# Kernel tuning notes

Hardware: AMD Instinct MI355X
Metric: run time of the kernel (lower is better)

The kernel has to match this reference:

```python
import jax, jax.numpy as jnp
import numpy as np

N = 2048
D_T = 256; D_F = 256
E_T = 32; E_F = 32; E_C = 128
C = 5; Q = 512


def setup_inputs() -> dict:
    key = jax.random.key(0)
    ks = jax.random.split(key, 12)
    # full graph minus self-loops, row-major (matches dense_to_sparse ordering)
    r, c = np.meshgrid(np.arange(N), np.arange(N), indexing='ij')
    m = r != c
    edge_index = jnp.asarray(np.stack([r[m], c[m]]), dtype=jnp.int32)  # [2, N*(N-1)]
    E = edge_index.shape[1]
    s = 0.02
    return {
        'time_features': jax.random.normal(ks[0], (N, D_T), jnp.float32),
        'edge_index': edge_index,
        'time_edge_weight': jax.random.uniform(ks[1], (E,), jnp.float32),
        'freq_features': jax.random.normal(ks[2], (N, D_F), jnp.float32),
        'freq_edge_weight': jax.random.uniform(ks[3], (E,), jnp.float32),
        'labels': jax.random.randint(ks[4], (N,), 0, C, jnp.int32),
        'num_classes': C,
        'query_size': Q,
        'Wt': jax.random.normal(ks[5], (D_T, E_T), jnp.float32) * s,
        'bt': jnp.zeros((E_T,), jnp.float32),
        'Wf': jax.random.normal(ks[6], (D_F, E_F), jnp.float32) * s,
        'bf': jnp.zeros((E_F,), jnp.float32),
        'Wc': jax.random.normal(ks[7], (E_T + E_F + C, E_C), jnp.float32) * s,
        'bc': jnp.zeros((E_C,), jnp.float32),
        'Wo': jax.random.normal(ks[8], (E_C, C), jnp.float32) * s,
        'bo': jnp.zeros((C,), jnp.float32),
    }


def _gcn(x, A, W, b):
    # torch_geometric GCNConv: D^{-1/2}(A + I)D^{-1/2} (X W) + b
    n = A.shape[0]
    Ah = A + jnp.eye(n, dtype=A.dtype)
    deg = Ah.sum(axis=1)
    dis = jnp.where(deg > 0, jax.lax.rsqrt(deg), 0.0)
    return (dis[:, None] * Ah * dis[None, :]) @ (x @ W) + b


def reference(time_features, edge_index, time_edge_weight, freq_features,
              freq_edge_weight, labels, num_classes, query_size,
              Wt, bt, Wf, bf, Wc, bc, Wo, bo):
    n = time_features.shape[0]
    lrelu = lambda z: jax.nn.leaky_relu(z, 0.01)

    def dense_adj(w):  # A[dst, src] = w
        return jnp.zeros((n, n), w.dtype).at[edge_index[1], edge_index[0]].add(w)

    te = lrelu(_gcn(time_features, dense_adj(time_edge_weight), Wt, bt))
    fe = lrelu(_gcn(freq_features, dense_adj(freq_edge_weight), Wf, bf))

    # to_one_hot: one_hot[:n - query_size, labels] = 1 -> support rows get 1 in
    # every column that appears anywhere in `labels`
    cols = jnp.zeros((num_classes,), te.dtype).at[labels].set(1.0)
    rowmask = (jnp.arange(n) < (n - query_size)).astype(te.dtype)
    one_hot = rowmask[:, None] * cols[None, :]

    feats = jnp.concatenate([te, fe, one_hot], axis=-1)  # [n, E_T+E_F+C]

    # graph_construction (no_grad in original): 1 / (L1 distance over the
    # non-one-hot dims + 1e-5), zero diagonal
    fd = jax.lax.stop_gradient(feats[:, : feats.shape[1] - num_classes])
    dist = jnp.sum(jnp.abs(fd[:, None, :] - fd[None, :, :]), axis=-1)  # [n, n]
    Aw = (1.0 / (dist + 1e-5)) * (1.0 - jnp.eye(n, dtype=feats.dtype))

    emb = lrelu(_gcn(feats, Aw, Wc, bc))
    return emb @ Wo + bo
```

## Files before the change

### kernel.cpp

```cpp
#include <hip/hip_runtime.h>
#include <hip/hip_bf16.h>

#define N 2048
#define NM1 2047
#define DT 256
#define ET 32
#define EC 128
#define NC 5
#define FS 80
#define FD 69
#define KC_ET 16
#define KC_EC 16

typedef __hip_bfloat16 bf16;

__global__ __launch_bounds__(256) void k_deg_label_xw(const float* __restrict__ tw,
                                                      const float* __restrict__ fw,
                                                      const int* __restrict__ labels,
                                                      const float* __restrict__ Xt,
                                                      const float* __restrict__ Wt,
                                                      const float* __restrict__ Xf,
                                                      const float* __restrict__ Wf,
                                                      float* __restrict__ degT,
                                                      float* __restrict__ degF,
                                                      float* __restrict__ cols,
                                                      float* __restrict__ Yt,
                                                      float* __restrict__ Yf){
    int b = blockIdx.x;
    int t = threadIdx.x;
    if (b < 512){
        int p = (b & 7)*256 + t;
        if (p >= NM1) return;
        int s0 = (b >> 3)*32;
        float lowT=0.f, highT=0.f, lowF=0.f, highF=0.f;
        #pragma unroll 8
        for (int r = 0; r < 32; ++r){
            int s = s0 + r;
            float vt = tw[(size_t)s*NM1 + p];
            float vf = fw[(size_t)s*NM1 + p];
            if (s <= p){ highT += vt; highF += vf; }
            else       { lowT  += vt; lowF  += vf; }
        }
        atomicAdd(&degT[p],   lowT);
        atomicAdd(&degF[p],   lowF);
        atomicAdd(&degT[p+1], highT);
        atomicAdd(&degF[p+1], highF);
        return;
    }
    if (b == 512){
        __shared__ float lc[NC];
        if (t < NC) lc[t] = 0.f;
        __syncthreads();
        for (int i = t; i < N; i += 256){
            int l = labels[i];
            if (l >= 0 && l < NC) lc[l] = 1.f;
        }
        __syncthreads();
        if (t < NC) cols[t] = lc[t];
        return;
    }
    int idx = b - 513;
    const float* X = (idx & 256) ? Xf : Xt;
    const float* W = (idx & 256) ? Wf : Wt;
    float*       Y = (idx & 256) ? Yf : Yt;
    __shared__ float Ws[DT*ET];
    __shared__ float Xs[8*DT];
    for (int j = t; j < DT*ET; j += 256) Ws[j] = W[j];
    int i0 = (idx & 255)*8;
    for (int j = t; j < 8*DT; j += 256) Xs[j] = X[(size_t)i0*DT + j];
    __syncthreads();
    int r = t >> 5, f = t & 31;
    const float* xr = Xs + r*DT;
    float acc = 0.f;
    #pragma unroll 8
    for (int d = 0; d < DT; ++d) acc += xr[d]*Ws[d*ET+f];
    Y[(size_t)(i0+r)*ET+f] = acc;
}

__global__ __launch_bounds__(256) void k_agg_et(const float* __restrict__ tw,
                                                const float* __restrict__ fw,
                                                const float* __restrict__ Yt,
                                                const float* __restrict__ Yf,
                                                const float* __restrict__ degT,
                                                const float* __restrict__ degF,
                                                float* __restrict__ Pt,
                                                float* __restrict__ Pf){
    __shared__ float Ast[64*68];
    __shared__ float Asf[64*68];
    __shared__ float Zst[64*ET];
    __shared__ float Zsf[64*ET];
    int t = threadIdx.x;
    int i0 = blockIdx.x*64;
    int kc = blockIdx.y;
    int k0 = kc*128;
    int g  = t >> 7;
    int tt = t & 127;
    int ig = tt >> 3, fg = tt & 7;
    int r0 = ig*4, c0 = fg*4;
    const float* As = g ? Asf : Ast;
    const float* Zs = g ? Zsf : Zst;
    float acc[4][4];
    #pragma unroll
    for (int u=0;u<4;++u)
        #pragma unroll
        for (int v=0;v<4;++v) acc[u][v]=0.f;

    for (int kt = 0; kt < 2; ++kt){
        int kb = k0 + kt*64;
        #pragma unroll
        for (int e = 0; e < 16; ++e){
            int id = t + e*256;
            int k_l = id >> 6, i_l = id & 63;
            int k = kb + k_l;
            int gi = i0 + i_l;
            float vt, vf;
            if (gi == k){ vt = 0.f; vf = 0.f; }
            else {
                size_t base = (size_t)k*NM1 + gi - (gi > k ? 1 : 0);
                vt = tw[base]; vf = fw[base];
            }
            Ast[k_l*68 + i_l] = vt;
            Asf[k_l*68 + i_l] = vf;
        }
        #pragma unroll
        for (int e = 0; e < 2; ++e){
            int id = t + e*256;
            int row = id >> 3;
            int c4  = (id & 7)*4;
            float rdT = rsqrtf(1.f + degT[kb+row]);
            float rdF = rsqrtf(1.f + degF[kb+row]);
            float4 yt = *(const float4*)&Yt[(size_t)(kb+row)*ET + c4];
            float4 yf = *(const float4*)&Yf[(size_t)(kb+row)*ET + c4];
            yt.x*=rdT; yt.y*=rdT; yt.z*=rdT; yt.w*=rdT;
            yf.x*=rdF; yf.y*=rdF; yf.z*=rdF; yf.w*=rdF;
            *(float4*)&Zst[row*ET + c4] = yt;
            *(float4*)&Zsf[row*ET + c4] = yf;
        }
        __syncthreads();
        for (int k = 0; k < 64; ++k){
            float4 a = *(const float4*)&As[k*68 + r0];
            float4 z = *(const float4*)&Zs[k*ET + c0];
            const float* ap = (const float*)&a;
            const float* zp = (const float*)&z;
            #pragma unroll
            for (int u = 0; u < 4; ++u)
                #pragma unroll
                for (int v = 0; v < 4; ++v)
                    acc[u][v] += ap[u]*zp[v];
        }
        __syncthreads();
    }
    float* P = g ? Pf : Pt;
    #pragma unroll
    for (int u = 0; u < 4; ++u){
        size_t ii = (size_t)(i0 + r0 + u);
        float4 o;
        float* po = (float*)&o;
        #pragma unroll
        for (int v = 0; v < 4; ++v) po[v]=acc[u][v];
        *(float4*)&P[(size_t)kc*(N*ET) + ii*ET + c0] = o;
    }
}

__global__ __launch_bounds__(256) void k_feats_epi(const float* __restrict__ Pt,
                                                   const float* __restrict__ Pf,
                                                   const float* __restrict__ Yt,
                                                   const float* __restrict__ Yf,
                                                   const float* __restrict__ degT,
                                                   const float* __restrict__ degF,
                                                   const float* __restrict__ bt,
                                                   const float* __restrict__ bfv,
                                                   const float* __restrict__ cols,
                                                   const int* __restrict__ qsize,
                                                   float* __restrict__ feats){
    int idx = blockIdx.x*256 + threadIdx.x;
    int i = idx >> 6;
    int f = idx & 63;
    float s, rd, b;
    if (f < ET){
        rd = rsqrtf(1.f + degT[i]);
        s = rd*Yt[(size_t)i*ET + f];
        #pragma unroll
        for (int kc = 0; kc < KC_ET; ++kc) s += Pt[(size_t)kc*(N*ET) + (size_t)i*ET + f];
        b = bt[f];
    } else {
        int g = f - ET;
        rd = rsqrtf(1.f + degF[i]);
        s = rd*Yf[(size_t)i*ET + g];
        #pragma unroll
        for (int kc = 0; kc < KC_ET; ++kc) s += Pf[(size_t)kc*(N*ET) + (size_t)i*ET + g];
        b = bfv[g];
    }
    float v = rd*s + b;
    feats[(size_t)i*FS + f] = v > 0.f ? v : 0.01f*v;
    if (f < NC){
        int nsup = N - qsize[0];
        feats[(size_t)i*FS + 2*ET + f] = (i < nsup) ? cols[f] : 0.f;
    }
}

__global__ __launch_bounds__(256) void k_build_aw(const float* __restrict__ feats,
                                                  float* __restrict__ Aw,
                                                  float* __restrict__ dsum){
    __shared__ float fiT[64*68];
    __shared__ float fjT[64*68];
    int t = threadIdx.x;
    int i0 = blockIdx.x*64, j0 = blockIdx.y*64;
    {
        int row = t >> 2;
        int cb  = (t & 3)*16;
        const float4* si = (const float4*)(feats + (size_t)(i0+row)*FS + cb);
        const float4* sj = (const float4*)(feats + (size_t)(j0+row)*FS + cb);
        #pragma unroll
        for (int s = 0; s < 4; ++s){
            float4 v = si[s];
            float4 w = sj[s];
            int c = cb + s*4;
            fiT[(c+0)*68+row]=v.x; fiT[(c+1)*68+row]=v.y; fiT[(c+2)*68+row]=v.z; fiT[(c+3)*68+row]=v.w;
            fjT[(c+0)*68+row]=w.x; fjT[(c+1)*68+row]=w.y; fjT[(c+2)*68+row]=w.z; fjT[(c+3)*68+row]=w.w;
        }
    }
    __syncthreads();
    int tx = t & 15, ty = t >> 4;
    float acc[4][4];
    #pragma unroll
    for (int u=0;u<4;++u)
        #pragma unroll
        for (int v=0;v<4;++v) acc[u][v]=0.f;
    for (int d = 0; d < 64; ++d){
        float4 a4 = *(const float4*)&fiT[d*68 + ty*4];
        float4 b4 = *(const float4*)&fjT[d*68 + tx*4];
        const float* ap = (const float*)&a4;
        const float* bp = (const float*)&b4;
        #pragma unroll
        for (int u = 0; u < 4; ++u)
            #pragma unroll
            for (int v = 0; v < 4; ++v)
                acc[u][v] += fabsf(ap[u]-bp[v]);
    }
    #pragma unroll
    for (int u = 0; u < 4; ++u){
        int gi = i0 + ty*4 + u;
        float4 o;
        float* po = (float*)&o;
        #pragma unroll
        for (int v = 0; v < 4; ++v){
            int gj = j0 + tx*4 + v;
            po[v] = (gi==gj) ? 1.0f : 1.0f/(acc[u][v] + 1e-5f);
        }
        *(float4*)&Aw[(size_t)gi*N + j0 + tx*4] = o;
        float rs = (po[0]+po[1]) + (po[2]+po[3]);
        rs += __shfl_xor(rs, 1);
        rs += __shfl_xor(rs, 2);
        rs += __shfl_xor(rs, 4);
        rs += __shfl_xor(rs, 8);
        if (tx == 0) atomicAdd(&dsum[gi], rs);
    }
}

__global__ __launch_bounds__(256) void k_featswc(const float* __restrict__ feats,
                                                 const float* __restrict__ Wc,
                                                 const float* __restrict__ dsum,
                                                 float* __restrict__ Zc){
    __shared__ float Wcs[FD*EC];
    __shared__ float fr[8][FD+3];
    int t = threadIdx.x;
    for (int idx = t; idx < FD*EC; idx += 256) Wcs[idx] = Wc[idx];
    int i0 = blockIdx.x*8;
    for (int idx = t; idx < 8*FD; idx += 256){
        int r = idx / FD;
        int c = idx - r*FD;
        fr[r][c] = feats[(size_t)(i0+r)*FS + c];
    }
    __syncthreads();
    int f  = t & 127;
    int rh = t >> 7;
    for (int rr = 0; rr < 4; ++rr){
        int r = rh*4 + rr;
        float acc = 0.f;
        #pragma unroll
        for (int d = 0; d < FD; ++d) acc += fr[r][d]*Wcs[d*EC+f];
        int i = i0 + r;
        Zc[(size_t)i*EC + f] = rsqrtf(dsum[i])*acc;
    }
}

__global__ __launch_bounds__(256) void k_agg_ec(const float* __restrict__ Aw,
                                                const float* __restrict__ Zc,
                                                float* __restrict__ Pe){
    __shared__ float As[64*68];
    __shared__ float Zs[64*128];
    int t = threadIdx.x;
    int i0 = blockIdx.x*64;
    int kc = blockIdx.y;
    int k0 = kc*128;
    int rg = t >> 4;
    int cg = t & 15;
    int r0 = rg*4;
    int ca = cg*4, cb = 64 + cg*4;
    float acc[4][8];
    #pragma unroll
    for (int u=0;u<4;++u)
        #pragma unroll
        for (int v=0;v<8;++v) acc[u][v]=0.f;

    for (int kt = 0; kt < 2; ++kt){
        int kb = k0 + kt*64;
        #pragma unroll
        for (int e = 0; e < 4; ++e){
            int id = t + e*256;
            int k_l = id >> 4;
            int i4  = (id & 15)*4;
            *(float4*)&As[k_l*68 + i4] = *(const float4*)&Aw[(size_t)(kb+k_l)*N + i0 + i4];
        }
        #pragma unroll
        for (int e = 0; e < 8; ++e){
            int id = t + e*256;
            int k_l = id >> 5;
            int c4  = (id & 31)*4;
            *(float4*)&Zs[k_l*128 + c4] = *(const float4*)&Zc[(size_t)(kb+k_l)*EC + c4];
        }
        __syncthreads();
        for (int k = 0; k < 64; ++k){
            float4 a  = *(const float4*)&As[k*68 + r0];
            float4 z0 = *(const float4*)&Zs[k*128 + ca];
            float4 z1 = *(const float4*)&Zs[k*128 + cb];
            float a4[4] = {a.x,a.y,a.z,a.w};
            float zl[4] = {z0.x,z0.y,z0.z,z0.w};
            float zh[4] = {z1.x,z1.y,z1.z,z1.w};
            #pragma unroll
            for (int u = 0; u < 4; ++u){
                #pragma unroll
                for (int v = 0; v < 4; ++v){
                    acc[u][v]   += a4[u]*zl[v];
                    acc[u][v+4] += a4[u]*zh[v];
                }
            }
        }
        __syncthreads();
    }
    #pragma unroll
    for (int u = 0; u < 4; ++u){
        size_t ii = (size_t)(i0 + r0 + u);
        float4 o0, o1;
        float* p0 = (float*)&o0; float* p1 = (float*)&o1;
        #pragma unroll
        for (int v = 0; v < 4; ++v){ p0[v]=acc[u][v]; p1[v]=acc[u][v+4]; }
        *(float4*)&Pe[(size_t)kc*(N*EC) + ii*EC + ca] = o0;
        *(float4*)&Pe[(size_t)kc*(N*EC) + ii*EC + cb] = o1;
    }
}

__global__ __launch_bounds__(256) void k_embfinal(const float* __restrict__ Pe,
                                                  const float* __restrict__ dsum,
                                                  const float* __restrict__ bc,
                                                  const float* __restrict__ Wo,
                                                  const float* __restrict__ bo,
                                                  float* __restrict__ out){
    __shared__ float vs[2][EC];
    __shared__ float Wos[EC*NC];
    __shared__ float bos[NC];
    int t = threadIdx.x;
    for (int idx = t; idx < EC*NC; idx += 256) Wos[idx] = Wo[idx];
    if (t < NC) bos[t] = bo[t];
    int rr = t >> 7, f = t & 127;
    int i = blockIdx.x*2 + rr;
    size_t idx = (size_t)i*EC + f;
    float s = 0.f;
    #pragma unroll
    for (int kc = 0; kc < KC_EC; ++kc) s += Pe[(size_t)kc*(N*EC) + idx];
    float v = rsqrtf(dsum[i])*s + bc[f];
    vs[rr][f] = v > 0.f ? v : 0.01f*v;
    __syncthreads();
    if (t < 2*NC){
        int r = t / NC;
        int c = t - r*NC;
        float a = bos[c];
        #pragma unroll 8
        for (int f2 = 0; f2 < EC; ++f2) a += vs[r][f2]*Wos[f2*NC+c];
        out[(size_t)(blockIdx.x*2 + r)*NC + c] = a;
    }
}

extern "C" void kernel_launch(void* const* d_in, const int* in_sizes, int n_in,
                              void* d_out, int out_size, void* d_ws, size_t ws_size,
                              hipStream_t stream) {
    const float* time_features = (const float*)d_in[0];
    const float* tw            = (const float*)d_in[2];
    const float* freq_features = (const float*)d_in[3];
    const float* fw            = (const float*)d_in[4];
    const int*   labels        = (const int*)d_in[5];
    const int*   qsize         = (const int*)d_in[7];
    const float* Wt  = (const float*)d_in[8];
    const float* bt  = (const float*)d_in[9];
    const float* Wf  = (const float*)d_in[10];
    const float* bfv = (const float*)d_in[11];
    const float* Wc  = (const float*)d_in[12];
    const float* bc  = (const float*)d_in[13];
    const float* Wo  = (const float*)d_in[14];
    const float* bo  = (const float*)d_in[15];
    float* out = (float*)d_out;

    float* ws    = (float*)d_ws;
    float* Yt    = ws;
    float* Yf    = Yt + (size_t)N*ET;
    float* Zc    = Yf + (size_t)N*ET;
    float* degT  = Zc + (size_t)N*EC;
    float* degF  = degT + N;
    float* dsum  = degF + N;
    float* colsb = dsum + N;
    float* feats = colsb + 8;
    float* Aw    = feats + (size_t)N*FS;
    float* Pt    = Aw + (size_t)N*N;
    float* Pf    = Pt + (size_t)KC_ET*N*ET;
    float* Pe    = Pf + (size_t)KC_ET*N*ET;

    hipMemsetAsync(degT, 0, 3*N*sizeof(float), stream);
    k_deg_label_xw<<<1025, 256, 0, stream>>>(tw, fw, labels,
                                             time_features, Wt, freq_features, Wf,
                                             degT, degF, colsb, Yt, Yf);
    k_agg_et<<<dim3(N/64, KC_ET), 256, 0, stream>>>(tw, fw, Yt, Yf, degT, degF, Pt, Pf);
    k_feats_epi<<<(N*64)/256, 256, 0, stream>>>(Pt, Pf, Yt, Yf, degT, degF,
                                                bt, bfv, colsb, qsize, feats);
    k_build_aw<<<dim3(N/64, N/64), 256, 0, stream>>>(feats, Aw, dsum);
    k_featswc<<<N/8, 256, 0, stream>>>(feats, Wc, dsum, Zc);
    k_agg_ec<<<dim3(N/64, KC_EC), 256, 0, stream>>>(Aw, Zc, Pe);
    k_embfinal<<<N/2, 256, 0, stream>>>(Pe, dsum, bc, Wo, bo, out);
}
```

Before: 207.3 us.

## Use split-bf16 MFMA for the Aw×Zc aggregation instead of scalar FP32 FMAs

The dense N×N by N×128 aggregation now runs on bf16 MFMA 16x16x32 instructions. Each FP32 operand is split into hi and lo bf16 parts, and three MFMAs per tile (hi·hi, lo·hi, hi·lo) recover near-FP32 accuracy. k_build_aw writes Aw as two bf16 planes, and k_featswc writes Zc transposed as bf16 hi/lo planes so the MFMA operands load contiguously along K. The intent is to replace the scalar FMA loop with matrix-core throughput. The cost is three MFMAs per product, the extra split-and-pack work, and a small loss of precision from dropping the lo·lo term.

```diff
diff --git a/kernel.cpp b/kernel.cpp
--- a/kernel.cpp
+++ b/kernel.cpp
@@ -13,6 +13,22 @@
 #define KC_EC 16
 
 typedef __hip_bfloat16 bf16;
+typedef unsigned short u16;
+typedef float f32x4 __attribute__((ext_vector_type(4)));
+typedef __bf16 bf16x8 __attribute__((ext_vector_type(8)));
+
+__device__ inline u16 bf16_rne(float x){
+    unsigned int b = __float_as_uint(x);
+    b += 0x7fffu + ((b >> 16) & 1u);
+    return (u16)(b >> 16);
+}
+__device__ inline float bf16_to_f(u16 h){
+    return __uint_as_float(((unsigned int)h) << 16);
+}
+
+__device__ inline f32x4 mfma16x16x32(bf16x8 a, bf16x8 b, f32x4 c){
+    return __builtin_amdgcn_mfma_f32_16x16x32_bf16(a, b, c, 0, 0, 0);
+}
 
 __global__ __launch_bounds__(256) void k_deg_label_xw(const float* __restrict__ tw,
                                                       const float* __restrict__ fw,
@@ -200,7 +216,8 @@
 }
 
 __global__ __launch_bounds__(256) void k_build_aw(const float* __restrict__ feats,
-                                                  float* __restrict__ Aw,
+                                                  u16* __restrict__ Aw_hi,
+                                                  u16* __restrict__ Aw_lo,
                                                   float* __restrict__ dsum){
     __shared__ float fiT[64*68];
     __shared__ float fjT[64*68];
@@ -241,14 +258,24 @@
     #pragma unroll
     for (int u = 0; u < 4; ++u){
         int gi = i0 + ty*4 + u;
-        float4 o;
-        float* po = (float*)&o;
+        float po[4];
+        u16 hh[4], ll[4];
         #pragma unroll
         for (int v = 0; v < 4; ++v){
             int gj = j0 + tx*4 + v;
-            po[v] = (gi==gj) ? 1.0f : 1.0f/(acc[u][v] + 1e-5f);
-        }
-        *(float4*)&Aw[(size_t)gi*N + j0 + tx*4] = o;
+            float w = (gi==gj) ? 1.0f : 1.0f/(acc[u][v] + 1e-5f);
+            po[v] = w;
+            u16 h = bf16_rne(w);
+            hh[v] = h;
+            ll[v] = bf16_rne(w - bf16_to_f(h));
+        }
+        uint2 ph, pl;
+        ph.x = (unsigned)hh[0] | ((unsigned)hh[1]<<16);
+        ph.y = (unsigned)hh[2] | ((unsigned)hh[3]<<16);
+        pl.x = (unsigned)ll[0] | ((unsigned)ll[1]<<16);
+        pl.y = (unsigned)ll[2] | ((unsigned)ll[3]<<16);
+        *(uint2*)&Aw_hi[(size_t)gi*N + j0 + tx*4] = ph;
+        *(uint2*)&Aw_lo[(size_t)gi*N + j0 + tx*4] = pl;
         float rs = (po[0]+po[1]) + (po[2]+po[3]);
         rs += __shfl_xor(rs, 1);
         rs += __shfl_xor(rs, 2);
@@ -261,9 +288,11 @@
 __global__ __launch_bounds__(256) void k_featswc(const float* __restrict__ feats,
                                                  const float* __restrict__ Wc,
                                                  const float* __restrict__ dsum,
-                                                 float* __restrict__ Zc){
+                                                 u16* __restrict__ ZcT_hi,
+                                                 u16* __restrict__ ZcT_lo){
     __shared__ float Wcs[FD*EC];
     __shared__ float fr[8][FD+3];
+    __shared__ float zb[128][12];
     int t = threadIdx.x;
     for (int idx = t; idx < FD*EC; idx += 256) Wcs[idx] = Wc[idx];
     int i0 = blockIdx.x*8;
@@ -281,73 +310,94 @@
         #pragma unroll
         for (int d = 0; d < FD; ++d) acc += fr[r][d]*Wcs[d*EC+f];
         int i = i0 + r;
-        Zc[(size_t)i*EC + f] = rsqrtf(dsum[i])*acc;
-    }
-}
-
-__global__ __launch_bounds__(256) void k_agg_ec(const float* __restrict__ Aw,
-                                                const float* __restrict__ Zc,
+        zb[f][r] = rsqrtf(dsum[i])*acc;
+    }
+    __syncthreads();
+    int p = rh, f2 = f;
+    float4 v0 = *(const float4*)&zb[f2][0];
+    float4 v1 = *(const float4*)&zb[f2][4];
+    float vv[8] = {v0.x, v0.y, v0.z, v0.w, v1.x, v1.y, v1.z, v1.w};
+    u16 s[8];
+    #pragma unroll
+    for (int j = 0; j < 8; ++j){
+        u16 h = bf16_rne(vv[j]);
+        s[j] = p ? bf16_rne(vv[j] - bf16_to_f(h)) : h;
+    }
+    uint4 pk;
+    pk.x = (unsigned)s[0] | ((unsigned)s[1]<<16);
+    pk.y = (unsigned)s[2] | ((unsigned)s[3]<<16);
+    pk.z = (unsigned)s[4] | ((unsigned)s[5]<<16);
+    pk.w = (unsigned)s[6] | ((unsigned)s[7]<<16);
+    u16* dst = p ? ZcT_lo : ZcT_hi;
+    *(uint4*)&dst[(size_t)f2*N + i0] = pk;
+}
+
+__global__ __launch_bounds__(256) void k_agg_ec(const u16* __restrict__ Aw_hi,
+                                                const u16* __restrict__ Aw_lo,
+                                                const u16* __restrict__ ZcT_hi,
+                                                const u16* __restrict__ ZcT_lo,
                                                 float* __restrict__ Pe){
-    __shared__ float As[64*68];
-    __shared__ float Zs[64*128];
-    int t = threadIdx.x;
+    __shared__ u16 Ah[64*72];
+    __shared__ u16 Al[64*72];
+    __shared__ u16 Zh[128*72];
+    __shared__ u16 Zl[128*72];
+    int t = threadIdx.x;
+    int w  = t >> 6;
+    int l  = t & 63;
+    int lr = l & 15;
+    int lg = l >> 4;
     int i0 = blockIdx.x*64;
-    int kc = blockIdx.y;
-    int k0 = kc*128;
-    int rg = t >> 4;
-    int cg = t & 15;
-    int r0 = rg*4;
-    int ca = cg*4, cb = 64 + cg*4;
-    float acc[4][8];
-    #pragma unroll
-    for (int u=0;u<4;++u)
-        #pragma unroll
-        for (int v=0;v<8;++v) acc[u][v]=0.f;
-
-    for (int kt = 0; kt < 2; ++kt){
-        int kb = k0 + kt*64;
+    int kb0 = blockIdx.y*128;
+    f32x4 acc[8];
+    #pragma unroll
+    for (int tt = 0; tt < 8; ++tt) acc[tt] = (f32x4){0.f, 0.f, 0.f, 0.f};
+
+    for (int sub = 0; sub < 2; ++sub){
+        int kbs = kb0 + sub*64;
+        #pragma unroll
+        for (int e = 0; e < 2; ++e){
+            int id = t + e*256;
+            int row = id >> 3, ch = (id & 7)*8;
+            uint4 vh = *(const uint4*)&Aw_hi[(size_t)(i0+row)*N + kbs + ch];
+            uint4 vl = *(const uint4*)&Aw_lo[(size_t)(i0+row)*N + kbs + ch];
+            *(uint4*)&Ah[row*72 + ch] = vh;
+            *(uint4*)&Al[row*72 + ch] = vl;
+        }
         #pragma unroll
         for (int e = 0; e < 4; ++e){
             int id = t + e*256;
-            int k_l = id >> 4;
-            int i4  = (id & 15)*4;
-            *(float4*)&As[k_l*68 + i4] = *(const float4*)&Aw[(size_t)(kb+k_l)*N + i0 + i4];
-        }
-        #pragma unroll
-        for (int e = 0; e < 8; ++e){
-            int id = t + e*256;
-            int k_l = id >> 5;
-            int c4  = (id & 31)*4;
-            *(float4*)&Zs[k_l*128 + c4] = *(const float4*)&Zc[(size_t)(kb+k_l)*EC + c4];
-        }
-        __syncthreads();
-        for (int k = 0; k < 64; ++k){
-            float4 a  = *(const float4*)&As[k*68 + r0];
-            float4 z0 = *(const float4*)&Zs[k*128 + ca];
-            float4 z1 = *(const float4*)&Zs[k*128 + cb];
-            float a4[4] = {a.x,a.y,a.z,a.w};
-            float zl[4] = {z0.x,z0.y,z0.z,z0.w};
-            float zh[4] = {z1.x,z1.y,z1.z,z1.w};
+            int row = id >> 3, ch = (id & 7)*8;
+            uint4 vh = *(const uint4*)&ZcT_hi[(size_t)row*N + kbs + ch];
+            uint4 vl = *(const uint4*)&ZcT_lo[(size_t)row*N + kbs + ch];
+            *(uint4*)&Zh[row*72 + ch] = vh;
+            *(uint4*)&Zl[row*72 + ch] = vl;
+        }
+        __syncthreads();
+        #pragma unroll
+        for (int ks = 0; ks < 2; ++ks){
+            int aoff = (w*16 + lr)*72 + ks*32 + lg*8;
+            bf16x8 aH = *(const bf16x8*)&Ah[aoff];
+            bf16x8 aL = *(const bf16x8*)&Al[aoff];
             #pragma unroll
-            for (int u = 0; u < 4; ++u){
-                #pragma unroll
-                for (int v = 0; v < 4; ++v){
-                    acc[u][v]   += a4[u]*zl[v];
-                    acc[u][v+4] += a4[u]*zh[v];
-                }
+            for (int tt = 0; tt < 8; ++tt){
+                int zoff = (tt*16 + lr)*72 + ks*32 + lg*8;
+                bf16x8 bH = *(const bf16x8*)&Zh[zoff];
+                bf16x8 bL = *(const bf16x8*)&Zl[zoff];
+                acc[tt] = mfma16x16x32(aH, bH, acc[tt]);
+                acc[tt] = mfma16x16x32(aL, bH, acc[tt]);
+                acc[tt] = mfma16x16x32(aH, bL, acc[tt]);
             }
         }
         __syncthreads();
     }
-    #pragma unroll
-    for (int u = 0; u < 4; ++u){
-        size_t ii = (size_t)(i0 + r0 + u);
-        float4 o0, o1;
-        float* p0 = (float*)&o0; float* p1 = (float*)&o1;
-        #pragma unroll
-        for (int v = 0; v < 4; ++v){ p0[v]=acc[u][v]; p1[v]=acc[u][v+4]; }
-        *(float4*)&Pe[(size_t)kc*(N*EC) + ii*EC + ca] = o0;
-        *(float4*)&Pe[(size_t)kc*(N*EC) + ii*EC + cb] = o1;
+    float* pout = Pe + (size_t)blockIdx.y*((size_t)N*EC);
+    #pragma unroll
+    for (int tt = 0; tt < 8; ++tt){
+        #pragma unroll
+        for (int r = 0; r < 4; ++r){
+            int gi = i0 + w*16 + lg*4 + r;
+            pout[(size_t)gi*EC + tt*16 + lr] = acc[tt][r];
+        }
     }
 }
 
@@ -415,6 +465,11 @@
     float* Pf    = Pt + (size_t)KC_ET*N*ET;
     float* Pe    = Pf + (size_t)KC_ET*N*ET;
 
+    u16* Aw_hi  = (u16*)Aw;
+    u16* Aw_lo  = Aw_hi + (size_t)N*N;
+    u16* ZcT_hi = (u16*)Zc;
+    u16* ZcT_lo = ZcT_hi + (size_t)N*EC;
+
     hipMemsetAsync(degT, 0, 3*N*sizeof(float), stream);
     k_deg_label_xw<<<1025, 256, 0, stream>>>(tw, fw, labels,
                                              time_features, Wt, freq_features, Wf,
@@ -422,8 +477,8 @@
     k_agg_et<<<dim3(N/64, KC_ET), 256, 0, stream>>>(tw, fw, Yt, Yf, degT, degF, Pt, Pf);
     k_feats_epi<<<(N*64)/256, 256, 0, stream>>>(Pt, Pf, Yt, Yf, degT, degF,
                                                 bt, bfv, colsb, qsize, feats);
-    k_build_aw<<<dim3(N/64, N/64), 256, 0, stream>>>(feats, Aw, dsum);
-    k_featswc<<<N/8, 256, 0, stream>>>(feats, Wc, dsum, Zc);
-    k_agg_ec<<<dim3(N/64, KC_EC), 256, 0, stream>>>(Aw, Zc, Pe);
+    k_build_aw<<<dim3(N/64, N/64), 256, 0, stream>>>(feats, Aw_hi, Aw_lo, dsum);
+    k_featswc<<<N/8, 256, 0, stream>>>(feats, Wc, dsum, ZcT_hi, ZcT_lo);
+    k_agg_ec<<<dim3(N/64, KC_EC), 256, 0, stream>>>(Aw_hi, Aw_lo, ZcT_hi, ZcT_lo, Pe);
     k_embfinal<<<N/2, 256, 0, stream>>>(Pe, dsum, bc, Wo, bo, out);
 }
```

Measured after the change: 199.8 us. 3.6% less time.
